# Performance work log

Hardware: AMD Instinct MI355X
Metric: run time of the kernel (lower is better)

## Reference

```python
import jax, jax.numpy as jnp
import numpy as np

T, B, D, H = 512, 64, 1024, 1024


def setup_inputs() -> dict:
    key = jax.random.key(0)
    k_x, k_wi, k_wh = jax.random.split(key, 3)
    scale_i = 1.0 / np.sqrt(D)
    scale_h = 1.0 / np.sqrt(H)
    return {
        "x": jax.random.normal(k_x, (T, B, D), dtype=jnp.float32),
        "c0": jnp.zeros((B, H), dtype=jnp.float32),
        "h0": jnp.zeros((B, H), dtype=jnp.float32),
        "Wi": jax.random.normal(k_wi, (D, 4 * H), dtype=jnp.float32) * scale_i,
        "Wh": jax.random.normal(k_wh, (H, 4 * H), dtype=jnp.float32) * scale_h,
        "b": jnp.zeros((4 * H,), dtype=jnp.float32),
    }


def reference(x, c0, h0, Wi, Wh, b):
    """LSTM recurrence over leading (time) axis, faithful to flax LSTMCell math.

    Gates: i = sigmoid, f = sigmoid, g = tanh, o = sigmoid;
    c' = f*c + i*g; h' = o*tanh(c'). Input projection has no bias, hidden
    projection carries the bias (matching flax LSTMCell). Returns ys = h per
    step, shape [T, B, H] (the scan outputs of the original module).
    """
    # Precompute the input-side gate projection for all timesteps at once
    # (one big GEMM instead of T small ones): [T, B, 4H]
    xg = jnp.einsum("tbd,dg->tbg", x, Wi)

    hdim = Wh.shape[0]

    def step(carry, xg_t):
        c, h = carry
        gates = xg_t + h @ Wh + b  # [B, 4H]
        i, f, g, o = jnp.split(gates, 4, axis=-1)
        i = jax.nn.sigmoid(i)
        f = jax.nn.sigmoid(f)
        g = jnp.tanh(g)
        o = jax.nn.sigmoid(o)
        c_new = f * c + i * g
        h_new = o * jnp.tanh(c_new)
        return (c_new, h_new), h_new

    (_, _), ys = jax.lax.scan(step, (c0, h0), xg)
    return ys  # [T, B, H]
```

## Files before the change

### kernel.cpp

```cpp
#include <hip/hip_runtime.h>
#include <hip/hip_bf16.h>


#define T_STEPS  512
#define BATCH    64
#define DIM      1024
#define NG       4096
#define NBLK     256
#define PTHREADS 512
#define HSLOT    ((size_t)(BATCH * DIM + 2048))

typedef __attribute__((ext_vector_type(8))) short frag8;
typedef __attribute__((ext_vector_type(4))) float f32x4;

__device__ __forceinline__ short f2bf(float f) {
    union { float f; unsigned u; } v; v.f = f;
    unsigned r = v.u + 0x7fffu + ((v.u >> 16) & 1u);
    return (short)(r >> 16);
}
__device__ __forceinline__ float sigm(float x) { return 1.0f / (1.0f + __expf(-x)); }
__device__ __forceinline__ float tanh_fast(float x) { return 1.0f - 2.0f / (__expf(2.0f * x) + 1.0f); }


__global__ __launch_bounds__(256)
void cast_transpose(const float* __restrict__ W, short* __restrict__ WT) {
    __shared__ float tile[32][33];
    int k0 = blockIdx.x * 32;
    int n0 = blockIdx.y * 32;
    int tx = threadIdx.x & 31, ty = threadIdx.x >> 5;
    #pragma unroll
    for (int i = 0; i < 32; i += 8)
        tile[ty + i][tx] = W[(size_t)(k0 + ty + i) * NG + n0 + tx];
    __syncthreads();
    #pragma unroll
    for (int i = 0; i < 32; i += 8)
        WT[(size_t)(n0 + ty + i) * DIM + k0 + tx] = f2bf(tile[tx][ty + i]);
}

__global__ __launch_bounds__(256)
void init_state(const float* __restrict__ c0, const float* __restrict__ h0,
                float* __restrict__ c, short* __restrict__ hring,
                unsigned* __restrict__ flags) {
    int i = blockIdx.x * 256 + threadIdx.x;
    c[i] = c0[i];
    hring[i] = f2bf(h0[i]);
    if (i < NBLK * 32) flags[i] = 0u;
}

__global__ __launch_bounds__(256)
void xcast(const float* __restrict__ x, short* __restrict__ xb, int n8) {
    int i = blockIdx.x * 256 + threadIdx.x;
    if (i >= n8) return;
    const float4* p = (const float4*)(x + (size_t)i * 8);
    float4 a = p[0], b = p[1];
    frag8 v;
    v[0] = f2bf(a.x); v[1] = f2bf(a.y); v[2] = f2bf(a.z); v[3] = f2bf(a.w);
    v[4] = f2bf(b.x); v[5] = f2bf(b.y); v[6] = f2bf(b.z); v[7] = f2bf(b.w);
    *(frag8*)(xb + (size_t)i * 8) = v;
}

__global__ __launch_bounds__(256)
void xgemm(const short* __restrict__ A, const short* __restrict__ B,
           float* __restrict__ CT_, int M) {
    __shared__ short As[4096];
    __shared__ short Bs[4096];
    const int tid = threadIdx.x;
    const int w = tid >> 6, l = tid & 63, m = l & 15, q = l >> 4;
    const size_t abase = (size_t)blockIdx.x * 128 * DIM;
    const size_t bbase = (size_t)blockIdx.y * 128 * DIM;

    f32x4 acc[2][8];
    #pragma unroll
    for (int i = 0; i < 2; ++i)
        #pragma unroll
        for (int j = 0; j < 8; ++j) acc[i][j] = (f32x4){0.f, 0.f, 0.f, 0.f};

    for (int kc = 0; kc < 32; ++kc) {
        #pragma unroll
        for (int c2 = 0; c2 < 2; ++c2) {
            int t2 = c2 * 256 + tid;
            int seg = t2 >> 7, row = t2 & 127;
            const short* ga = A + abase + (size_t)row * DIM + kc * 32 + seg * 8;
            const short* gb = B + bbase + (size_t)row * DIM + kc * 32 + seg * 8;
            __builtin_amdgcn_global_load_lds(
                (const __attribute__((address_space(1))) void*)ga,
                (__attribute__((address_space(3))) void*)(As + t2 * 8), 16, 0, 0);
            __builtin_amdgcn_global_load_lds(
                (const __attribute__((address_space(1))) void*)gb,
                (__attribute__((address_space(3))) void*)(Bs + t2 * 8), 16, 0, 0);
        }
        __syncthreads();
        frag8 a0 = *(const frag8*)(As + (q * 128 + w * 32 + m) * 8);
        frag8 a1 = *(const frag8*)(As + (q * 128 + w * 32 + 16 + m) * 8);
        #pragma unroll
        for (int nt = 0; nt < 8; ++nt) {
            frag8 bf = *(const frag8*)(Bs + (q * 128 + nt * 16 + m) * 8);
            acc[0][nt] = __builtin_amdgcn_mfma_f32_16x16x32_bf16(a0, bf, acc[0][nt], 0, 0, 0);
            acc[1][nt] = __builtin_amdgcn_mfma_f32_16x16x32_bf16(a1, bf, acc[1][nt], 0, 0, 0);
        }
        __syncthreads();
    }
    #pragma unroll
    for (int mt = 0; mt < 2; ++mt)
        #pragma unroll
        for (int nt = 0; nt < 8; ++nt) {
            int row0 = blockIdx.x * 128 + w * 32 + mt * 16 + q * 4;
            int col  = blockIdx.y * 128 + nt * 16 + m;
            *(float4*)(CT_ + (size_t)col * M + row0) =
                make_float4(acc[mt][nt][0], acc[mt][nt][1], acc[mt][nt][2], acc[mt][nt][3]);
        }
}

__global__ __launch_bounds__(PTHREADS)
void lstm_persist(const float* __restrict__ xgT,
                  const short* __restrict__ WhT,
                  const float* __restrict__ bias,
                  float* __restrict__ cstate,
                  short* __restrict__ hring,
                  float* __restrict__ y,
                  unsigned* __restrict__ flags,
                  int gstep0, int CTC, int M) {
    __shared__ short whs[2048 * 8];
    __shared__ float gsm2[2][64][17];
    const int tid = threadIdx.x;
    const int w = tid >> 6, l = tid & 63, m = l & 15, q4 = l >> 4;
    const int bt = w & 3, kh = w >> 2;
    const int j0 = blockIdx.x * 4;

    for (int idx = tid; idx < 2048; idx += PTHREADS) {
        int kcc = idx >> 6, ll = idx & 63, cc = ll & 15, qq = ll >> 4;
        int gcol = (cc >> 2) * DIM + j0 + (cc & 3);
        *(frag8*)(whs + idx * 8) =
            *(const frag8*)(WhT + (size_t)gcol * DIM + kcc * 32 + qq * 8);
    }

    const int eb = tid >> 2, ej = tid & 3;
    float creg = 0.f, bv0 = 0.f, bv1 = 0.f, bv2 = 0.f, bv3 = 0.f;
    if (tid < 256) {
        creg = cstate[eb * DIM + j0 + ej];
        bv0 = bias[0 * DIM + j0 + ej];
        bv1 = bias[1 * DIM + j0 + ej];
        bv2 = bias[2 * DIM + j0 + ej];
        bv3 = bias[3 * DIM + j0 + ej];
    }
    __syncthreads();

    for (int t = 0; t < CTC; ++t) {
        float xv0 = 0.f, xv1 = 0.f, xv2 = 0.f, xv3 = 0.f;
        if (tid < 256) {
            const size_t r = (size_t)t * BATCH + eb;
            xv0 = xgT[(size_t)(0 * DIM + j0 + ej) * M + r];
            xv1 = xgT[(size_t)(1 * DIM + j0 + ej) * M + r];
            xv2 = xgT[(size_t)(2 * DIM + j0 + ej) * M + r];
            xv3 = xgT[(size_t)(3 * DIM + j0 + ej) * M + r];
        }

        if (t > 0 && w == 0) {
            const unsigned target = (unsigned)(gstep0 + t);
            for (;;) {
                bool ok = true;
                #pragma unroll
                for (int i = 0; i < 4; ++i) {
                    unsigned f = __hip_atomic_load(&flags[(l * 4 + i) * 32],
                        __ATOMIC_RELAXED, __HIP_MEMORY_SCOPE_AGENT);
                    ok &= (f >= target);
                }
                if (__all(ok)) break;
                __builtin_amdgcn_s_sleep(2);
            }
        }
        __syncthreads();

        const short* hrow = hring + (size_t)t * HSLOT
                          + (size_t)(bt * 16 + m) * DIM + kh * 512;
        f32x4 acc = {0.f, 0.f, 0.f, 0.f};
        #pragma unroll
        for (int kc = 0; kc < 16; ++kc) {
            frag8 a = *(const frag8*)(hrow + kc * 32 + q4 * 8);
            frag8 b = *(const frag8*)(whs + ((kh * 16 + kc) * 64 + l) * 8);
            acc = __builtin_amdgcn_mfma_f32_16x16x32_bf16(a, b, acc, 0, 0, 0);
        }
        #pragma unroll
        for (int r = 0; r < 4; ++r)
            gsm2[kh][bt * 16 + q4 * 4 + r][m] = acc[r];
        __syncthreads();

        if (tid < 256) {
            const float gi = sigm(     gsm2[0][eb][ej]      + gsm2[1][eb][ej]      + xv0 + bv0);
            const float gf = sigm(     gsm2[0][eb][4 + ej]  + gsm2[1][eb][4 + ej]  + xv1 + bv1);
            const float gg = tanh_fast(gsm2[0][eb][8 + ej]  + gsm2[1][eb][8 + ej]  + xv2 + bv2);
            const float go = sigm(     gsm2[0][eb][12 + ej] + gsm2[1][eb][12 + ej] + xv3 + bv3);
            creg = gf * creg + gi * gg;
            const float hn = go * tanh_fast(creg);

            const float y1 = __shfl_down(hn, 1), y2 = __shfl_down(hn, 2), y3 = __shfl_down(hn, 3);
            if (ej == 0)
                *(float4*)(y + ((size_t)t * BATCH + eb) * DIM + j0) = make_float4(hn, y1, y2, y3);

            unsigned hb0 = (unsigned)(unsigned short)f2bf(hn);
            unsigned hb1 = __shfl_down(hb0, 1);
            unsigned hb2 = __shfl_down(hb0, 2);
            unsigned hb3 = __shfl_down(hb0, 3);
            if (ej == 0) {
                const int dslot = (t == CTC - 1) ? 0 : (t + 1);
                unsigned long long v = (unsigned long long)(hb0 | (hb1 << 16))
                                     | ((unsigned long long)(hb2 | (hb3 << 16)) << 32);
                __hip_atomic_store(
                    (unsigned long long*)(hring + (size_t)dslot * HSLOT + eb * DIM + j0),
                    v, __ATOMIC_RELAXED, __HIP_MEMORY_SCOPE_AGENT);
            }
        }

        if (t < CTC - 1) {
            asm volatile("s_waitcnt vmcnt(0)" ::: "memory");
            __syncthreads();
            if (tid == 0)
                __hip_atomic_store(&flags[blockIdx.x * 32], (unsigned)(gstep0 + t + 1),
                                   __ATOMIC_RELAXED, __HIP_MEMORY_SCOPE_AGENT);
        }
    }
    if (tid < 256) cstate[eb * DIM + j0 + ej] = creg;
}

extern "C" void kernel_launch(void* const* d_in, const int* in_sizes, int n_in,
                              void* d_out, int out_size, void* d_ws, size_t ws_size,
                              hipStream_t stream) {
    const float* x  = (const float*)d_in[0];
    const float* c0 = (const float*)d_in[1];
    const float* h0 = (const float*)d_in[2];
    const float* Wi = (const float*)d_in[3];
    const float* Wh = (const float*)d_in[4];
    const float* b  = (const float*)d_in[5];
    float* out = (float*)d_out;

    char* ws = (char*)d_ws;
    short*    WiT   = (short*)(ws);
    short*    WhT   = (short*)(ws + 8388608);
    float*    c     = (float*)(ws + 16777216);
    unsigned* flags = (unsigned*)(ws + 17039360);
    const size_t fixed = 17072128;

    const size_t perCT = HSLOT * 2 + 131072 + 1048576;
    int CT = 2;
    const int cands[9] = {512, 256, 128, 64, 32, 16, 8, 4, 2};
    for (int i = 0; i < 9; ++i)
        if (fixed + (size_t)cands[i] * perCT <= ws_size) { CT = cands[i]; break; }

    short* hring = (short*)(ws + fixed);
    short* xbf   = (short*)(ws + fixed + (size_t)CT * HSLOT * 2);
    float* xgT   = (float*)(ws + fixed + (size_t)CT * (HSLOT * 2 + 131072));
    const int M = CT * BATCH;

    cast_transpose<<<dim3(DIM / 32, NG / 32), 256, 0, stream>>>(Wi, WiT);
    cast_transpose<<<dim3(DIM / 32, NG / 32), 256, 0, stream>>>(Wh, WhT);
    init_state<<<dim3(BATCH * DIM / 256), 256, 0, stream>>>(c0, h0, c, hring, flags);

    const int nchunks = T_STEPS / CT;
    for (int ch = 0; ch < nchunks; ++ch) {
        const size_t xoff = (size_t)ch * CT * BATCH * DIM;
        const int n8 = CT * BATCH * DIM / 8;
        xcast<<<dim3((n8 + 255) / 256), 256, 0, stream>>>(x + xoff, xbf, n8);
        xgemm<<<dim3(M / 128, NG / 128), 256, 0, stream>>>(xbf, WiT, xgT, M);
        lstm_persist<<<dim3(NBLK), PTHREADS, 0, stream>>>(
            xgT, WhT, b, c, hring, out + xoff, flags, ch * CT, CT, M);
    }
}
```

Before: 4.274 ms.

## Repartition persistent LSTM by batch groups with register-resident Wh and local sync

Reworks the persistent LSTM kernel so each of the 256 blocks owns a 16-row batch group and 16 hidden columns, and each wave owns 4 columns over the full K range. The Wh slice is held in registers instead of LDS, the gate exchange happens through wave shuffles rather than a shared-memory reduction with an extra barrier, and each block waits only on the 64 flags of its own batch group instead of all 256 blocks. The aim is to cut per-step synchronization latency and LDS traffic on the serial recurrence. The cost is heavy register pressure from 32 frag8 weight registers and a longer per-wave MFMA chain with no K split.

```diff
diff --git a/kernel.cpp b/kernel.cpp
--- a/kernel.cpp
+++ b/kernel.cpp
@@ -7,7 +7,9 @@
 #define DIM      1024
 #define NG       4096
 #define NBLK     256
-#define PTHREADS 512
+#define PTHREADS 256
+#define GBLK     64
+#define GB       16
 #define HSLOT    ((size_t)(BATCH * DIM + 2048))
 
 typedef __attribute__((ext_vector_type(8))) short frag8;
@@ -111,7 +113,7 @@
         }
 }
 
-__global__ __launch_bounds__(PTHREADS)
+__global__ __launch_bounds__(PTHREADS, 1)
 void lstm_persist(const float* __restrict__ xgT,
                   const short* __restrict__ WhT,
                   const float* __restrict__ bias,
@@ -120,95 +122,86 @@
                   float* __restrict__ y,
                   unsigned* __restrict__ flags,
                   int gstep0, int CTC, int M) {
-    __shared__ short whs[2048 * 8];
-    __shared__ float gsm2[2][64][17];
     const int tid = threadIdx.x;
-    const int w = tid >> 6, l = tid & 63, m = l & 15, q4 = l >> 4;
-    const int bt = w & 3, kh = w >> 2;
-    const int j0 = blockIdx.x * 4;
-
-    for (int idx = tid; idx < 2048; idx += PTHREADS) {
-        int kcc = idx >> 6, ll = idx & 63, cc = ll & 15, qq = ll >> 4;
-        int gcol = (cc >> 2) * DIM + j0 + (cc & 3);
-        *(frag8*)(whs + idx * 8) =
-            *(const frag8*)(WhT + (size_t)gcol * DIM + kcc * 32 + qq * 8);
-    }
-
-    const int eb = tid >> 2, ej = tid & 3;
-    float creg = 0.f, bv0 = 0.f, bv1 = 0.f, bv2 = 0.f, bv3 = 0.f;
-    if (tid < 256) {
-        creg = cstate[eb * DIM + j0 + ej];
-        bv0 = bias[0 * DIM + j0 + ej];
-        bv1 = bias[1 * DIM + j0 + ej];
-        bv2 = bias[2 * DIM + j0 + ej];
-        bv3 = bias[3 * DIM + j0 + ej];
-    }
-    __syncthreads();
+    const int w = tid >> 6, l = tid & 63;
+    const int m = l & 15, q4 = l >> 4;
+    const int grp  = blockIdx.x >> 6;
+    const int kblk = blockIdx.x & 63;
+    const int j0w  = kblk * 16 + w * 4;
+    const int gcol = (m >> 2) * DIM + j0w + (m & 3);
+
+    frag8 wreg[32];
+    #pragma unroll
+    for (int kc = 0; kc < 32; ++kc)
+        wreg[kc] = *(const frag8*)(WhT + (size_t)gcol * DIM + kc * 32 + q4 * 8);
+
+    const int eb = grp * GB + (l >> 2);
+    const int ec = j0w + (l & 3);
+    float creg = cstate[(size_t)eb * DIM + ec];
+    const float bv = bias[gcol];
+
+    const int rsel  = (l >> 2) & 3;
+    const int sbase = (l & 48) + (l & 3);
 
     for (int t = 0; t < CTC; ++t) {
-        float xv0 = 0.f, xv1 = 0.f, xv2 = 0.f, xv3 = 0.f;
-        if (tid < 256) {
-            const size_t r = (size_t)t * BATCH + eb;
-            xv0 = xgT[(size_t)(0 * DIM + j0 + ej) * M + r];
-            xv1 = xgT[(size_t)(1 * DIM + j0 + ej) * M + r];
-            xv2 = xgT[(size_t)(2 * DIM + j0 + ej) * M + r];
-            xv3 = xgT[(size_t)(3 * DIM + j0 + ej) * M + r];
-        }
+        const float4 xv = *(const float4*)(
+            xgT + (size_t)gcol * M + (size_t)t * BATCH + grp * GB + q4 * 4);
 
         if (t > 0 && w == 0) {
             const unsigned target = (unsigned)(gstep0 + t);
+            const unsigned* fp = &flags[(grp * GBLK + l) * 32];
             for (;;) {
-                bool ok = true;
-                #pragma unroll
-                for (int i = 0; i < 4; ++i) {
-                    unsigned f = __hip_atomic_load(&flags[(l * 4 + i) * 32],
-                        __ATOMIC_RELAXED, __HIP_MEMORY_SCOPE_AGENT);
-                    ok &= (f >= target);
-                }
-                if (__all(ok)) break;
+                unsigned f = __hip_atomic_load(fp, __ATOMIC_RELAXED,
+                                               __HIP_MEMORY_SCOPE_AGENT);
+                if (__all(f >= target)) break;
                 __builtin_amdgcn_s_sleep(2);
             }
         }
         __syncthreads();
 
         const short* hrow = hring + (size_t)t * HSLOT
-                          + (size_t)(bt * 16 + m) * DIM + kh * 512;
+                          + (size_t)(grp * GB + m) * DIM;
         f32x4 acc = {0.f, 0.f, 0.f, 0.f};
         #pragma unroll
-        for (int kc = 0; kc < 16; ++kc) {
+        for (int kc = 0; kc < 32; ++kc) {
             frag8 a = *(const frag8*)(hrow + kc * 32 + q4 * 8);
-            frag8 b = *(const frag8*)(whs + ((kh * 16 + kc) * 64 + l) * 8);
-            acc = __builtin_amdgcn_mfma_f32_16x16x32_bf16(a, b, acc, 0, 0, 0);
-        }
-        #pragma unroll
-        for (int r = 0; r < 4; ++r)
-            gsm2[kh][bt * 16 + q4 * 4 + r][m] = acc[r];
-        __syncthreads();
-
-        if (tid < 256) {
-            const float gi = sigm(     gsm2[0][eb][ej]      + gsm2[1][eb][ej]      + xv0 + bv0);
-            const float gf = sigm(     gsm2[0][eb][4 + ej]  + gsm2[1][eb][4 + ej]  + xv1 + bv1);
-            const float gg = tanh_fast(gsm2[0][eb][8 + ej]  + gsm2[1][eb][8 + ej]  + xv2 + bv2);
-            const float go = sigm(     gsm2[0][eb][12 + ej] + gsm2[1][eb][12 + ej] + xv3 + bv3);
-            creg = gf * creg + gi * gg;
-            const float hn = go * tanh_fast(creg);
-
-            const float y1 = __shfl_down(hn, 1), y2 = __shfl_down(hn, 2), y3 = __shfl_down(hn, 3);
-            if (ej == 0)
-                *(float4*)(y + ((size_t)t * BATCH + eb) * DIM + j0) = make_float4(hn, y1, y2, y3);
-
-            unsigned hb0 = (unsigned)(unsigned short)f2bf(hn);
-            unsigned hb1 = __shfl_down(hb0, 1);
-            unsigned hb2 = __shfl_down(hb0, 2);
-            unsigned hb3 = __shfl_down(hb0, 3);
-            if (ej == 0) {
-                const int dslot = (t == CTC - 1) ? 0 : (t + 1);
-                unsigned long long v = (unsigned long long)(hb0 | (hb1 << 16))
-                                     | ((unsigned long long)(hb2 | (hb3 << 16)) << 32);
-                __hip_atomic_store(
-                    (unsigned long long*)(hring + (size_t)dslot * HSLOT + eb * DIM + j0),
-                    v, __ATOMIC_RELAXED, __HIP_MEMORY_SCOPE_AGENT);
-            }
+            acc = __builtin_amdgcn_mfma_f32_16x16x32_bf16(a, wreg[kc], acc, 0, 0, 0);
+        }
+        acc[0] += xv.x + bv; acc[1] += xv.y + bv;
+        acc[2] += xv.z + bv; acc[3] += xv.w + bv;
+
+        float pre[4];
+        #pragma unroll
+        for (int g = 0; g < 4; ++g) {
+            const int src = sbase + g * 4;
+            float t0 = __shfl(acc[0], src);
+            float t1 = __shfl(acc[1], src);
+            float t2 = __shfl(acc[2], src);
+            float t3 = __shfl(acc[3], src);
+            pre[g] = rsel == 0 ? t0 : rsel == 1 ? t1 : rsel == 2 ? t2 : t3;
+        }
+        const float gi = sigm(pre[0]);
+        const float gf = sigm(pre[1]);
+        const float gg = tanh_fast(pre[2]);
+        const float go = sigm(pre[3]);
+        creg = gf * creg + gi * gg;
+        const float hn = go * tanh_fast(creg);
+
+        const float y1 = __shfl_down(hn, 1), y2 = __shfl_down(hn, 2), y3 = __shfl_down(hn, 3);
+        unsigned hb0 = (unsigned)(unsigned short)f2bf(hn);
+        unsigned hb1 = __shfl_down(hb0, 1);
+        unsigned hb2 = __shfl_down(hb0, 2);
+        unsigned hb3 = __shfl_down(hb0, 3);
+        if ((l & 3) == 0) {
+            *(float4*)(y + ((size_t)t * BATCH + eb) * DIM + j0w) =
+                make_float4(hn, y1, y2, y3);
+            const int dslot = (t == CTC - 1) ? 0 : (t + 1);
+            unsigned long long v = (unsigned long long)(hb0 | (hb1 << 16))
+                                 | ((unsigned long long)(hb2 | (hb3 << 16)) << 32);
+            __hip_atomic_store(
+                (unsigned long long*)(hring + (size_t)dslot * HSLOT
+                                      + (size_t)eb * DIM + j0w),
+                v, __ATOMIC_RELAXED, __HIP_MEMORY_SCOPE_AGENT);
         }
 
         if (t < CTC - 1) {
@@ -219,7 +212,7 @@
                                    __ATOMIC_RELAXED, __HIP_MEMORY_SCOPE_AGENT);
         }
     }
-    if (tid < 256) cstate[eb * DIM + j0 + ej] = creg;
+    cstate[(size_t)eb * DIM + ec] = creg;
 }
 
 extern "C" void kernel_launch(void* const* d_in, const int* in_sizes, int n_in,
```

Result: slower. 4.863 ms (+13.8%).

## Partition persistent LSTM blocks into independent batch groups with group-local flag sync

Applied to the files above, without the earlier changes.

Splits the 256 persistent blocks into 4 batch groups of 64 blocks. Each block now owns 16 hidden columns for 16 batch rows instead of 4 columns for all 64 rows, so a block only waits on the 64 flags of its own group rather than all 256. Each block now keeps four times as many Wh columns in shared memory, and the gate and index layouts are reworked to match. The y output store is moved after the flag publish so it leaves the critical path. The cost is more LDS per block and reading the h slice for only 16 batch rows.

```diff
diff --git a/kernel.cpp b/kernel.cpp
--- a/kernel.cpp
+++ b/kernel.cpp
@@ -8,6 +8,9 @@
 #define NG       4096
 #define NBLK     256
 #define PTHREADS 512
+#define NGRP     4
+#define GBLK     64
+#define GB       16
 #define HSLOT    ((size_t)(BATCH * DIM + 2048))
 
 typedef __attribute__((ext_vector_type(8))) short frag8;
@@ -111,7 +114,7 @@
         }
 }
 
-__global__ __launch_bounds__(PTHREADS)
+__global__ __launch_bounds__(PTHREADS, 1)
 void lstm_persist(const float* __restrict__ xgT,
                   const short* __restrict__ WhT,
                   const float* __restrict__ bias,
@@ -120,28 +123,34 @@
                   float* __restrict__ y,
                   unsigned* __restrict__ flags,
                   int gstep0, int CTC, int M) {
-    __shared__ short whs[2048 * 8];
-    __shared__ float gsm2[2][64][17];
+    __shared__ short whs[4 * 32 * 64 * 8];
+    __shared__ float gsm2[2][16][68];
     const int tid = threadIdx.x;
     const int w = tid >> 6, l = tid & 63, m = l & 15, q4 = l >> 4;
-    const int bt = w & 3, kh = w >> 2;
-    const int j0 = blockIdx.x * 4;
-
-    for (int idx = tid; idx < 2048; idx += PTHREADS) {
-        int kcc = idx >> 6, ll = idx & 63, cc = ll & 15, qq = ll >> 4;
-        int gcol = (cc >> 2) * DIM + j0 + (cc & 3);
+    const int cg = w & 3, kh = w >> 2;
+    const int grp  = blockIdx.x >> 6;
+    const int kblk = blockIdx.x & 63;
+    const int j0   = kblk * 16;
+
+    for (int idx = tid; idx < 4 * 32 * 64; idx += PTHREADS) {
+        int scg = idx >> 11, rem = idx & 2047;
+        int kcc = rem >> 6, ll = rem & 63, cc = ll & 15, qq = ll >> 4;
+        int gcol = (cc >> 2) * DIM + j0 + scg * 4 + (cc & 3);
         *(frag8*)(whs + idx * 8) =
             *(const frag8*)(WhT + (size_t)gcol * DIM + kcc * 32 + qq * 8);
     }
 
-    const int eb = tid >> 2, ej = tid & 3;
+    const int bl = l & 15;
+    const int jl = w * 4 + q4;
+    const int eb = grp * GB + bl;
+    const int ec = j0 + jl;
     float creg = 0.f, bv0 = 0.f, bv1 = 0.f, bv2 = 0.f, bv3 = 0.f;
     if (tid < 256) {
-        creg = cstate[eb * DIM + j0 + ej];
-        bv0 = bias[0 * DIM + j0 + ej];
-        bv1 = bias[1 * DIM + j0 + ej];
-        bv2 = bias[2 * DIM + j0 + ej];
-        bv3 = bias[3 * DIM + j0 + ej];
+        creg = cstate[(size_t)eb * DIM + ec];
+        bv0 = bias[0 * DIM + ec];
+        bv1 = bias[1 * DIM + ec];
+        bv2 = bias[2 * DIM + ec];
+        bv3 = bias[3 * DIM + ec];
     }
     __syncthreads();
 
@@ -149,65 +158,63 @@
         float xv0 = 0.f, xv1 = 0.f, xv2 = 0.f, xv3 = 0.f;
         if (tid < 256) {
             const size_t r = (size_t)t * BATCH + eb;
-            xv0 = xgT[(size_t)(0 * DIM + j0 + ej) * M + r];
-            xv1 = xgT[(size_t)(1 * DIM + j0 + ej) * M + r];
-            xv2 = xgT[(size_t)(2 * DIM + j0 + ej) * M + r];
-            xv3 = xgT[(size_t)(3 * DIM + j0 + ej) * M + r];
+            xv0 = xgT[(size_t)(0 * DIM + ec) * M + r];
+            xv1 = xgT[(size_t)(1 * DIM + ec) * M + r];
+            xv2 = xgT[(size_t)(2 * DIM + ec) * M + r];
+            xv3 = xgT[(size_t)(3 * DIM + ec) * M + r];
         }
 
         if (t > 0 && w == 0) {
             const unsigned target = (unsigned)(gstep0 + t);
+            const unsigned* fp = &flags[(grp * GBLK + l) * 32];
             for (;;) {
-                bool ok = true;
-                #pragma unroll
-                for (int i = 0; i < 4; ++i) {
-                    unsigned f = __hip_atomic_load(&flags[(l * 4 + i) * 32],
-                        __ATOMIC_RELAXED, __HIP_MEMORY_SCOPE_AGENT);
-                    ok &= (f >= target);
-                }
-                if (__all(ok)) break;
-                __builtin_amdgcn_s_sleep(2);
+                unsigned f = __hip_atomic_load(fp, __ATOMIC_RELAXED,
+                                               __HIP_MEMORY_SCOPE_AGENT);
+                if (__all(f >= target)) break;
+                __builtin_amdgcn_s_sleep(1);
             }
         }
         __syncthreads();
 
         const short* hrow = hring + (size_t)t * HSLOT
-                          + (size_t)(bt * 16 + m) * DIM + kh * 512;
+                          + (size_t)(grp * GB + m) * DIM + kh * 512;
         f32x4 acc = {0.f, 0.f, 0.f, 0.f};
         #pragma unroll
         for (int kc = 0; kc < 16; ++kc) {
             frag8 a = *(const frag8*)(hrow + kc * 32 + q4 * 8);
-            frag8 b = *(const frag8*)(whs + ((kh * 16 + kc) * 64 + l) * 8);
+            frag8 b = *(const frag8*)(whs + ((cg * 32 + kh * 16 + kc) * 64 + l) * 8);
             acc = __builtin_amdgcn_mfma_f32_16x16x32_bf16(a, b, acc, 0, 0, 0);
         }
         #pragma unroll
         for (int r = 0; r < 4; ++r)
-            gsm2[kh][bt * 16 + q4 * 4 + r][m] = acc[r];
-        __syncthreads();
-
+            gsm2[kh][q4 * 4 + r][(m >> 2) * 16 + cg * 4 + (m & 3)] = acc[r];
+        __syncthreads();
+
+        float hn = 0.f, ya = 0.f, yb = 0.f, yc = 0.f;
+        unsigned long long hv = 0ull;
         if (tid < 256) {
-            const float gi = sigm(     gsm2[0][eb][ej]      + gsm2[1][eb][ej]      + xv0 + bv0);
-            const float gf = sigm(     gsm2[0][eb][4 + ej]  + gsm2[1][eb][4 + ej]  + xv1 + bv1);
-            const float gg = tanh_fast(gsm2[0][eb][8 + ej]  + gsm2[1][eb][8 + ej]  + xv2 + bv2);
-            const float go = sigm(     gsm2[0][eb][12 + ej] + gsm2[1][eb][12 + ej] + xv3 + bv3);
+            const float gi = sigm(     gsm2[0][bl][ 0 + jl] + gsm2[1][bl][ 0 + jl] + xv0 + bv0);
+            const float gf = sigm(     gsm2[0][bl][16 + jl] + gsm2[1][bl][16 + jl] + xv1 + bv1);
+            const float gg = tanh_fast(gsm2[0][bl][32 + jl] + gsm2[1][bl][32 + jl] + xv2 + bv2);
+            const float go = sigm(     gsm2[0][bl][48 + jl] + gsm2[1][bl][48 + jl] + xv3 + bv3);
             creg = gf * creg + gi * gg;
-            const float hn = go * tanh_fast(creg);
-
-            const float y1 = __shfl_down(hn, 1), y2 = __shfl_down(hn, 2), y3 = __shfl_down(hn, 3);
-            if (ej == 0)
-                *(float4*)(y + ((size_t)t * BATCH + eb) * DIM + j0) = make_float4(hn, y1, y2, y3);
-
+            hn = go * tanh_fast(creg);
+
+            ya = __shfl(hn, bl + 16);
+            yb = __shfl(hn, bl + 32);
+            yc = __shfl(hn, bl + 48);
             unsigned hb0 = (unsigned)(unsigned short)f2bf(hn);
-            unsigned hb1 = __shfl_down(hb0, 1);
-            unsigned hb2 = __shfl_down(hb0, 2);
-            unsigned hb3 = __shfl_down(hb0, 3);
-            if (ej == 0) {
+            unsigned hb1 = __shfl(hb0, bl + 16);
+            unsigned hb2 = __shfl(hb0, bl + 32);
+            unsigned hb3 = __shfl(hb0, bl + 48);
+            if (l < 16) {
                 const int dslot = (t == CTC - 1) ? 0 : (t + 1);
-                unsigned long long v = (unsigned long long)(hb0 | (hb1 << 16))
-                                     | ((unsigned long long)(hb2 | (hb3 << 16)) << 32);
+                hv = (unsigned long long)(hb0 | (hb1 << 16))
+                   | ((unsigned long long)(hb2 | (hb3 << 16)) << 32);
                 __hip_atomic_store(
-                    (unsigned long long*)(hring + (size_t)dslot * HSLOT + eb * DIM + j0),
-                    v, __ATOMIC_RELAXED, __HIP_MEMORY_SCOPE_AGENT);
+                    (unsigned long long*)(hring + (size_t)dslot * HSLOT
+                                          + (size_t)eb * DIM + j0 + w * 4),
+                    hv, __ATOMIC_RELAXED, __HIP_MEMORY_SCOPE_AGENT);
             }
         }
 
@@ -218,8 +225,12 @@
                 __hip_atomic_store(&flags[blockIdx.x * 32], (unsigned)(gstep0 + t + 1),
                                    __ATOMIC_RELAXED, __HIP_MEMORY_SCOPE_AGENT);
         }
-    }
-    if (tid < 256) cstate[eb * DIM + j0 + ej] = creg;
+
+        if (tid < 256 && l < 16)
+            *(float4*)(y + ((size_t)t * BATCH + eb) * DIM + j0 + w * 4) =
+                make_float4(hn, ya, yb, yc);
+    }
+    if (tid < 256) cstate[(size_t)eb * DIM + ec] = creg;
 }
 
 extern "C" void kernel_launch(void* const* d_in, const int* in_sizes, int n_in,
```

After: 4.130 ms. 1.04x faster.
